# Performance work log

Hardware: AMD Instinct MI355X
Metric: run time of the kernel (lower is better)

The kernel has to match this reference:

```python
import jax, jax.numpy as jnp
import numpy as np

N_NODES = 50000
N_EDGES = 800000
IN_DIM = 128
HID_DIM = 256
OUT_DIM = 2


def setup_inputs() -> dict:
    key = jax.random.key(0)
    k = jax.random.split(key, 8)
    x = jax.random.normal(k[0], (N_NODES, IN_DIM), dtype=jnp.float32)
    edge_index = jax.random.randint(k[1], (2, N_EDGES), 0, N_NODES, dtype=jnp.int64)
    # Linear params (PyTorch-style fan-in scaling)
    W1 = jax.random.normal(k[2], (IN_DIM, HID_DIM), dtype=jnp.float32) / np.sqrt(IN_DIM)
    b1 = jnp.zeros((HID_DIM,), dtype=jnp.float32)
    W2 = jax.random.normal(k[3], (HID_DIM, OUT_DIM), dtype=jnp.float32) / np.sqrt(HID_DIM)
    b2 = jnp.zeros((OUT_DIM,), dtype=jnp.float32)
    # learnable GIN epsilons (init 0, as in PyG GINConv train_eps)
    eps1 = jnp.zeros((), dtype=jnp.float32)
    eps2 = jnp.zeros((), dtype=jnp.float32)
    return {"x": x, "edge_index": edge_index, "W1": W1, "b1": b1,
            "W2": W2, "b2": b2, "eps1": eps1, "eps2": eps2}


def _gin_conv(h, src, dst, num_nodes, eps, W, b):
    # aggregate: sum of neighbor features (scatter-add over edges)
    agg = jax.ops.segment_sum(h[src], dst, num_segments=num_nodes)  # [N, D]
    return ((1.0 + eps) * h + agg) @ W + b


def reference(x, edge_index, W1, b1, W2, b2, eps1, eps2):
    src, dst = edge_index[0], edge_index[1]
    n = x.shape[0]
    h = _gin_conv(x, src, dst, n, eps1, W1, b1)   # [N, HID]
    h = jax.nn.relu(h)
    out = _gin_conv(h, src, dst, n, eps2, W2, b2)  # [N, OUT]
    return out
```

## Files before the change

kernel.cpp:

```cpp
#include <hip/hip_runtime.h>

#define N_NODES 50000
#define N_EDGES 800000
#define IN_DIM 128
#define HID_DIM 256
#define OUT_DIM 2
#define CAP 64
#define NBKT 196
#define BCAP 6144
#define CHUNK 4096
#define POISON 0xAAAAAAAAu

typedef __attribute__((ext_vector_type(8))) short bh8;
typedef __attribute__((ext_vector_type(4))) float f4;
typedef __attribute__((ext_vector_type(4))) unsigned u4;

__device__ inline unsigned bf16rne(float f) {
    unsigned u = __float_as_uint(f);
    return (u + 0x7fffu + ((u >> 16) & 1u)) >> 16;
}
__device__ inline unsigned pack2(float lo, float hi) {
    return (bf16rne(hi) << 16) | bf16rne(lo);
}

__global__ __launch_bounds__(256) void k_prep_bin(
    const float* __restrict__ x, const float* __restrict__ W1,
    const int* __restrict__ ei,
    unsigned* __restrict__ xb, unsigned* __restrict__ W1p,
    unsigned* __restrict__ ccur, unsigned* __restrict__ coarse)
{
    __shared__ unsigned stage[CHUNK];
    __shared__ int hist[256], base[256], gpos[256], cur2[256];
    __shared__ int s_red[4];
    const int tid = threadIdx.x, lane = tid & 63, wv = tid >> 6;
    const int gtid = blockIdx.x * 256 + tid;
    const int gsz  = gridDim.x * 256;

    for (int i = gtid; i < 800000; i += gsz) {
        float4 a = ((const float4*)x)[2 * i];
        float4 b = ((const float4*)x)[2 * i + 1];
        u4 w;
        w[0] = pack2(a.x, a.y);
        w[1] = pack2(a.z, a.w);
        w[2] = pack2(b.x, b.y);
        w[3] = pack2(b.z, b.w);
        ((u4*)xb)[i] = w;
    }
    if (gtid < 16384) {
        int j = gtid;
        int d = j & 3, l = (j >> 2) & 63, s = (j >> 8) & 3, t = j >> 10;
        int k = 32 * s + 8 * (l >> 4) + 2 * d;
        int n = 16 * t + (l & 15);
        W1p[j] = (bf16rne(W1[(size_t)(k + 1) * HID_DIM + n]) << 16)
               |  bf16rne(W1[(size_t)k * HID_DIM + n]);
    }
    const int bid = blockIdx.x;
    if (bid >= NBKT) return;
    const int ebase = bid * CHUNK;
    const int ecnt  = min(CHUNK, N_EDGES - ebase);

    hist[tid] = 0;
    __syncthreads();
    int myd[16], mys[16];
#pragma unroll
    for (int r = 0; r < 16; r++) {
        int li = r * 256 + tid;
        if (li < ecnt) {
            int e = ebase + li;
            myd[r] = ei[N_EDGES + e];
            mys[r] = ei[e];
            atomicAdd(&hist[myd[r] >> 8], 1);
        } else myd[r] = -1;
    }
    __syncthreads();
    {
        int v = hist[tid], s = v;
#pragma unroll
        for (int off = 1; off < 64; off <<= 1) {
            int t = __shfl_up(s, off, 64);
            if (lane >= off) s += t;
        }
        if (lane == 63) s_red[wv] = s;
        __syncthreads();
        int wexcl = 0;
        for (int w = 0; w < wv; w++) wexcl += s_red[w];
        base[tid] = wexcl + s - v;
        cur2[tid] = 0;
        __syncthreads();
    }
    if (tid < NBKT && hist[tid] > 0) {
        atomicCAS(&ccur[tid], POISON, 0u);
        gpos[tid] = (int)atomicAdd(&ccur[tid], (unsigned)hist[tid]);
    }
    __syncthreads();
#pragma unroll
    for (int r = 0; r < 16; r++) {
        if (myd[r] >= 0) {
            int b = myd[r] >> 8;
            int pos = atomicAdd(&cur2[b], 1);
            stage[base[b] + pos] = ((unsigned)myd[r] << 16) | (unsigned)mys[r];
        }
    }
    __syncthreads();
    for (int i = tid; i < ecnt; i += 256) {
        unsigned rec = stage[i];
        int b = (int)(rec >> 24);
        int idx = gpos[b] + (i - base[b]);
        if (idx < BCAP) coarse[(size_t)b * BCAP + idx] = rec;
    }
}

__global__ __launch_bounds__(256) void k_fine(
    const unsigned* __restrict__ ccur, const unsigned* __restrict__ coarse,
    int* __restrict__ slots, int* __restrict__ cnt)
{
    __shared__ int cur[256];
    const int tid = threadIdx.x, bid = blockIdx.x;
    cur[tid] = 0;
    __syncthreads();
    const int cb = min((int)ccur[bid], BCAP);
    for (int i = tid; i < cb; i += 256) {
        unsigned rec = coarse[(size_t)bid * BCAP + i];
        int dst = (int)(rec >> 16);
        int src = (int)(rec & 0xffffu);
        int pos = atomicAdd(&cur[dst & 255], 1);
        if (pos < CAP) slots[(size_t)dst * CAP + pos] = src;
    }
    __syncthreads();
    int node = bid * 256 + tid;
    if (node < N_NODES) cnt[node] = min(cur[tid], CAP);
}

__global__ __launch_bounds__(256, 4) void k_gin1(
    const unsigned* __restrict__ xb,
    const int* __restrict__ cnt, const int* __restrict__ slots,
    const unsigned* __restrict__ W1p, const float* __restrict__ b1,
    const float* __restrict__ W2, const float* __restrict__ b2,
    const float* __restrict__ eps1p, const float* __restrict__ eps2p,
    float* __restrict__ p, float* __restrict__ out)
{
    __shared__ unsigned z[16 * 68];
    const int tid = threadIdx.x, lane = tid & 63, wv = tid >> 6;
    const int node0 = blockIdx.x * 16;
    const int nodeb = node0 + 4 * wv;
    const float e1 = 1.0f + eps1p[0];

    const int4 c4 = *(const int4*)(cnt + nodeb);
    int cns[4] = { min(c4.x, CAP), min(c4.y, CAP), min(c4.z, CAP), min(c4.w, CAP) };
    int srcs[4];
#pragma unroll
    for (int nn = 0; nn < 4; nn++) {
        srcs[nn] = slots[(size_t)(nodeb + nn) * CAP + ((lane < cns[nn]) ? lane : 0)];
    }
    unsigned us[4];
#pragma unroll
    for (int nn = 0; nn < 4; nn++)
        us[nn] = xb[(size_t)(nodeb + nn) * 64 + lane];
#pragma unroll
    for (int nn = 0; nn < 4; nn++)
        if (cns[nn] == 0) srcs[nn] = 0;

    unsigned u[4][16];
#pragma unroll
    for (int nn = 0; nn < 4; nn++) {
        int cn = cns[nn];
#pragma unroll
        for (int g = 0; g < 16; g++) {
            int sq = __shfl(srcs[nn], (g < cn) ? g : 0, 64);
            u[nn][g] = xb[(size_t)sq * 64 + lane];
        }
    }

#pragma unroll
    for (int nn = 0; nn < 4; nn++) {
        int cn = cns[nn];
        float ax = 0.f, ay = 0.f;
#pragma unroll
        for (int g = 0; g < 16; g++) {
            if (g < cn) {
                ax += __uint_as_float(u[nn][g] << 16);
                ay += __uint_as_float(u[nn][g] & 0xffff0000u);
            }
        }
        for (int j0 = 16; j0 < cn; j0 += 16) {
#pragma unroll
            for (int g = 0; g < 16; g++) {
                int idx = j0 + g;
                int sq = __shfl(srcs[nn], (idx < cn) ? idx : 0, 64);
                u[nn][g] = xb[(size_t)sq * 64 + lane];
            }
#pragma unroll
            for (int g = 0; g < 16; g++) {
                if (j0 + g < cn) {
                    ax += __uint_as_float(u[nn][g] << 16);
                    ay += __uint_as_float(u[nn][g] & 0xffff0000u);
                }
            }
        }
        ax = fmaf(e1, __uint_as_float(us[nn] << 16), ax);
        ay = fmaf(e1, __uint_as_float(us[nn] & 0xffff0000u), ay);
        z[(4 * wv + nn) * 68 + lane] = (bf16rne(ay) << 16) | bf16rne(ax);
    }
    __syncthreads();
    if (wv != 0) return;

    const int q = lane >> 4, c = lane & 15;
    bh8 afrag[4];
#pragma unroll
    for (int s = 0; s < 4; s++)
        afrag[s] = *(const bh8*)&z[c * 68 + 16 * s + 4 * q];

    f4 acc[16];
#pragma unroll
    for (int t = 0; t < 16; t++) acc[t] = (f4){0.f, 0.f, 0.f, 0.f};
#pragma unroll
    for (int t = 0; t < 16; t++) {
#pragma unroll
        for (int s = 0; s < 4; s++) {
            bh8 bfrag = *(const bh8*)(W1p + ((size_t)(t * 4 + s) * 64 + lane) * 4);
            acc[t] = __builtin_amdgcn_mfma_f32_16x16x32_bf16(afrag[s], bfrag, acc[t], 0, 0, 0);
        }
    }

    const float e2 = 1.0f + eps2p[0];
    float pxr[4] = {0.f, 0.f, 0.f, 0.f};
    float pyr[4] = {0.f, 0.f, 0.f, 0.f};
#pragma unroll
    for (int t = 0; t < 16; t++) {
        int n = 16 * t + c;
        float bb = b1[n];
        float2 w2 = *(const float2*)(W2 + (size_t)n * OUT_DIM);
#pragma unroll
        for (int r = 0; r < 4; r++) {
            float h = fmaxf(acc[t][r] + bb, 0.f);
            pxr[r] = fmaf(h, w2.x, pxr[r]);
            pyr[r] = fmaf(h, w2.y, pyr[r]);
        }
    }
#pragma unroll
    for (int off = 1; off < 16; off <<= 1) {
#pragma unroll
        for (int r = 0; r < 4; r++) {
            pxr[r] += __shfl_xor(pxr[r], off, 64);
            pyr[r] += __shfl_xor(pyr[r], off, 64);
        }
    }
    if (c == 0) {
        float2 b2v = *(const float2*)b2;
#pragma unroll
        for (int r = 0; r < 4; r++) {
            int node = node0 + q * 4 + r;
            *(float2*)(p + (size_t)node * OUT_DIM) = make_float2(pxr[r], pyr[r]);
            float2 o;
            o.x = fmaf(e2, pxr[r], b2v.x);
            o.y = fmaf(e2, pyr[r], b2v.y);
            *(float2*)(out + (size_t)node * OUT_DIM) = o;
        }
    }
}

__global__ __launch_bounds__(256) void k_out(
    const int* __restrict__ cnt, const int* __restrict__ slots,
    const float* __restrict__ p, float* __restrict__ out)
{
    const int tid = threadIdx.x, lane = tid & 63, wv = tid >> 6;
    const int node = blockIdx.x * 32 + wv * 8 + (lane >> 3);
    const int l = lane & 7;
    float sx = 0.f, sy = 0.f;
    if (node < N_NODES) {
        int cn = min(cnt[node], CAP);
        for (int j = l; j < cn; j += 8) {
            int src = slots[node * CAP + j];
            float2 v = *(const float2*)(p + (size_t)src * OUT_DIM);
            sx += v.x; sy += v.y;
        }
    }
#pragma unroll
    for (int off = 1; off <= 4; off <<= 1) {
        sx += __shfl_xor(sx, off, 64);
        sy += __shfl_xor(sy, off, 64);
    }
    if (l == 0 && node < N_NODES) {
        float2 o = *(const float2*)(out + (size_t)node * OUT_DIM);
        o.x += sx; o.y += sy;
        *(float2*)(out + (size_t)node * OUT_DIM) = o;
    }
}

extern "C" void kernel_launch(void* const* d_in, const int* in_sizes, int n_in,
                              void* d_out, int out_size, void* d_ws, size_t ws_size,
                              hipStream_t stream)
{
    (void)in_sizes; (void)n_in; (void)out_size; (void)ws_size;
    const float* x    = (const float*)d_in[0];
    const int*   ei   = (const int*)d_in[1];
    const float* W1   = (const float*)d_in[2];
    const float* b1   = (const float*)d_in[3];
    const float* W2   = (const float*)d_in[4];
    const float* b2   = (const float*)d_in[5];
    const float* eps1 = (const float*)d_in[6];
    const float* eps2 = (const float*)d_in[7];
    float* out = (float*)d_out;

    int* cnt         = (int*)d_ws;
    int* slots       = cnt + 50048;
    float* p         = (float*)(slots + 3200000);
    unsigned* xb     = (unsigned*)(p + 100000);
    unsigned* W1p    = xb + 3200000;
    unsigned* ccur   = (unsigned*)(W1p + 16384);
    unsigned* coarse = ccur + 256;

    k_prep_bin<<<2048, 256, 0, stream>>>(x, W1, ei, xb, W1p, ccur, coarse);
    k_fine<<<NBKT, 256, 0, stream>>>(ccur, coarse, slots, cnt);
    k_gin1<<<(N_NODES + 15) / 16, 256, 0, stream>>>(xb, cnt, slots,
                                                    W1p, b1, W2, b2,
                                                    eps1, eps2, p, out);
    k_out<<<(N_NODES + 31) / 32, 256, 0, stream>>>(cnt, slots, p, out);
}
```

Before: 173.3 us.

## Restructure GIN gather to 16-lane node groups and split MFMA across waves

The gather in k_gin1 now assigns 16 lanes per node, so each wave handles 4 nodes at once with 16-byte vector loads of the bf16 features, instead of looping over nodes with 4-byte loads per lane. The first-layer matmul is split so all four waves each compute a quarter of the hidden columns, rather than wave 0 doing all of it, and the partial second-layer projections are reduced through shared memory. k_fine switches to 1024-thread blocks and loads its bucket records into registers up front. Together these aim to raise memory-level parallelism in the gather and balance the matrix work across waves, at the cost of an extra block barrier and more register pressure.

```diff
diff --git a/kernel.cpp b/kernel.cpp
--- a/kernel.cpp
+++ b/kernel.cpp
@@ -110,25 +110,37 @@
     }
 }
 
-__global__ __launch_bounds__(256) void k_fine(
+__global__ __launch_bounds__(1024) void k_fine(
     const unsigned* __restrict__ ccur, const unsigned* __restrict__ coarse,
     int* __restrict__ slots, int* __restrict__ cnt)
 {
     __shared__ int cur[256];
     const int tid = threadIdx.x, bid = blockIdx.x;
-    cur[tid] = 0;
+    if (tid < 256) cur[tid] = 0;
     __syncthreads();
     const int cb = min((int)ccur[bid], BCAP);
-    for (int i = tid; i < cb; i += 256) {
-        unsigned rec = coarse[(size_t)bid * BCAP + i];
-        int dst = (int)(rec >> 16);
-        int src = (int)(rec & 0xffffu);
-        int pos = atomicAdd(&cur[dst & 255], 1);
-        if (pos < CAP) slots[(size_t)dst * CAP + pos] = src;
-    }
-    __syncthreads();
-    int node = bid * 256 + tid;
-    if (node < N_NODES) cnt[node] = min(cur[tid], CAP);
+    unsigned recs[6];
+#pragma unroll
+    for (int r = 0; r < 6; r++) {
+        int i = tid + r * 1024;
+        if (i < cb) recs[r] = coarse[(size_t)bid * BCAP + i];
+    }
+#pragma unroll
+    for (int r = 0; r < 6; r++) {
+        int i = tid + r * 1024;
+        if (i < cb) {
+            unsigned rec = recs[r];
+            int dst = (int)(rec >> 16);
+            int src = (int)(rec & 0xffffu);
+            int pos = atomicAdd(&cur[dst & 255], 1);
+            if (pos < CAP) slots[(size_t)dst * CAP + pos] = src;
+        }
+    }
+    __syncthreads();
+    if (tid < 256) {
+        int node = bid * 256 + tid;
+        if (node < N_NODES) cnt[node] = min(cur[tid], CAP);
+    }
 }
 
 __global__ __launch_bounds__(256, 4) void k_gin1(
@@ -139,70 +151,75 @@
     const float* __restrict__ eps1p, const float* __restrict__ eps2p,
     float* __restrict__ p, float* __restrict__ out)
 {
-    __shared__ unsigned z[16 * 68];
+    __shared__ __attribute__((aligned(16))) unsigned z[16 * 68];
+    __shared__ float2 pp[64];
     const int tid = threadIdx.x, lane = tid & 63, wv = tid >> 6;
     const int node0 = blockIdx.x * 16;
-    const int nodeb = node0 + 4 * wv;
+    const int sub = lane & 15;
+    const int grp = lane >> 4;
+    const int gb  = lane & 48;
+    const int node = node0 + 4 * wv + grp;
     const float e1 = 1.0f + eps1p[0];
-
-    const int4 c4 = *(const int4*)(cnt + nodeb);
-    int cns[4] = { min(c4.x, CAP), min(c4.y, CAP), min(c4.z, CAP), min(c4.w, CAP) };
-    int srcs[4];
-#pragma unroll
-    for (int nn = 0; nn < 4; nn++) {
-        srcs[nn] = slots[(size_t)(nodeb + nn) * CAP + ((lane < cns[nn]) ? lane : 0)];
-    }
-    unsigned us[4];
-#pragma unroll
-    for (int nn = 0; nn < 4; nn++)
-        us[nn] = xb[(size_t)(nodeb + nn) * 64 + lane];
-#pragma unroll
-    for (int nn = 0; nn < 4; nn++)
-        if (cns[nn] == 0) srcs[nn] = 0;
-
-    unsigned u[4][16];
-#pragma unroll
-    for (int nn = 0; nn < 4; nn++) {
-        int cn = cns[nn];
+    const u4* __restrict__ xb4 = (const u4*)xb;
+
+    const int cn = min(cnt[node], CAP);
+    int s1 = 0;
+    if (sub < cn) s1 = slots[(size_t)node * CAP + sub];
+
+    u4 us = xb4[(unsigned)(node * 16 + sub)];
+
+    u4 u[16];
+#pragma unroll
+    for (int g = 0; g < 16; g++) {
+        int sq = __shfl(s1, gb + g, 64);
+        u[g] = xb4[(unsigned)(sq * 16 + sub)];
+    }
+    float ax[8];
+#pragma unroll
+    for (int k = 0; k < 8; k++) ax[k] = 0.f;
+#pragma unroll
+    for (int g = 0; g < 16; g++) {
+        if (g < cn) {
+#pragma unroll
+            for (int k2 = 0; k2 < 4; k2++) {
+                unsigned w = u[g][k2];
+                ax[2 * k2]     += __uint_as_float(w << 16);
+                ax[2 * k2 + 1] += __uint_as_float(w & 0xffff0000u);
+            }
+        }
+    }
+    int j0 = 16;
+    while (__any(cn > j0)) {
+        int idx = j0 + sub;
+        int s2 = (idx < cn) ? slots[(size_t)node * CAP + idx] : 0;
+        u4 ut[16];
 #pragma unroll
         for (int g = 0; g < 16; g++) {
-            int sq = __shfl(srcs[nn], (g < cn) ? g : 0, 64);
-            u[nn][g] = xb[(size_t)sq * 64 + lane];
-        }
-    }
-
-#pragma unroll
-    for (int nn = 0; nn < 4; nn++) {
-        int cn = cns[nn];
-        float ax = 0.f, ay = 0.f;
+            int sq = __shfl(s2, gb + g, 64);
+            ut[g] = xb4[(unsigned)(sq * 16 + sub)];
+        }
 #pragma unroll
         for (int g = 0; g < 16; g++) {
-            if (g < cn) {
-                ax += __uint_as_float(u[nn][g] << 16);
-                ay += __uint_as_float(u[nn][g] & 0xffff0000u);
-            }
-        }
-        for (int j0 = 16; j0 < cn; j0 += 16) {
-#pragma unroll
-            for (int g = 0; g < 16; g++) {
-                int idx = j0 + g;
-                int sq = __shfl(srcs[nn], (idx < cn) ? idx : 0, 64);
-                u[nn][g] = xb[(size_t)sq * 64 + lane];
-            }
-#pragma unroll
-            for (int g = 0; g < 16; g++) {
-                if (j0 + g < cn) {
-                    ax += __uint_as_float(u[nn][g] << 16);
-                    ay += __uint_as_float(u[nn][g] & 0xffff0000u);
+            if (j0 + g < cn) {
+#pragma unroll
+                for (int k2 = 0; k2 < 4; k2++) {
+                    unsigned w = ut[g][k2];
+                    ax[2 * k2]     += __uint_as_float(w << 16);
+                    ax[2 * k2 + 1] += __uint_as_float(w & 0xffff0000u);
                 }
             }
         }
-        ax = fmaf(e1, __uint_as_float(us[nn] << 16), ax);
-        ay = fmaf(e1, __uint_as_float(us[nn] & 0xffff0000u), ay);
-        z[(4 * wv + nn) * 68 + lane] = (bf16rne(ay) << 16) | bf16rne(ax);
-    }
-    __syncthreads();
-    if (wv != 0) return;
+        j0 += 16;
+    }
+    u4 zw;
+#pragma unroll
+    for (int k2 = 0; k2 < 4; k2++) {
+        float lx = fmaf(e1, __uint_as_float(us[k2] << 16),         ax[2 * k2]);
+        float ly = fmaf(e1, __uint_as_float(us[k2] & 0xffff0000u), ax[2 * k2 + 1]);
+        zw[k2] = pack2(lx, ly);
+    }
+    *(u4*)&z[(4 * wv + grp) * 68 + 4 * sub] = zw;
+    __syncthreads();
 
     const int q = lane >> 4, c = lane & 15;
     bh8 afrag[4];
@@ -210,15 +227,16 @@
     for (int s = 0; s < 4; s++)
         afrag[s] = *(const bh8*)&z[c * 68 + 16 * s + 4 * q];
 
-    f4 acc[16];
-#pragma unroll
-    for (int t = 0; t < 16; t++) acc[t] = (f4){0.f, 0.f, 0.f, 0.f};
-#pragma unroll
-    for (int t = 0; t < 16; t++) {
+    f4 acc[4];
+#pragma unroll
+    for (int t = 0; t < 4; t++) acc[t] = (f4){0.f, 0.f, 0.f, 0.f};
+#pragma unroll
+    for (int tp = 0; tp < 4; tp++) {
+        int t = 4 * wv + tp;
 #pragma unroll
         for (int s = 0; s < 4; s++) {
             bh8 bfrag = *(const bh8*)(W1p + ((size_t)(t * 4 + s) * 64 + lane) * 4);
-            acc[t] = __builtin_amdgcn_mfma_f32_16x16x32_bf16(afrag[s], bfrag, acc[t], 0, 0, 0);
+            acc[tp] = __builtin_amdgcn_mfma_f32_16x16x32_bf16(afrag[s], bfrag, acc[tp], 0, 0, 0);
         }
     }
 
@@ -226,13 +244,13 @@
     float pxr[4] = {0.f, 0.f, 0.f, 0.f};
     float pyr[4] = {0.f, 0.f, 0.f, 0.f};
 #pragma unroll
-    for (int t = 0; t < 16; t++) {
-        int n = 16 * t + c;
+    for (int tp = 0; tp < 4; tp++) {
+        int n = 16 * (4 * wv + tp) + c;
         float bb = b1[n];
         float2 w2 = *(const float2*)(W2 + (size_t)n * OUT_DIM);
 #pragma unroll
         for (int r = 0; r < 4; r++) {
-            float h = fmaxf(acc[t][r] + bb, 0.f);
+            float h = fmaxf(acc[tp][r] + bb, 0.f);
             pxr[r] = fmaf(h, w2.x, pxr[r]);
             pyr[r] = fmaf(h, w2.y, pyr[r]);
         }
@@ -246,16 +264,26 @@
         }
     }
     if (c == 0) {
+#pragma unroll
+        for (int r = 0; r < 4; r++)
+            pp[wv * 16 + q * 4 + r] = make_float2(pxr[r], pyr[r]);
+    }
+    __syncthreads();
+
+    if (tid < 16) {
+        float px = 0.f, py = 0.f;
+#pragma unroll
+        for (int w = 0; w < 4; w++) {
+            float2 v = pp[w * 16 + tid];
+            px += v.x; py += v.y;
+        }
+        int nd = node0 + tid;
+        *(float2*)(p + (size_t)nd * OUT_DIM) = make_float2(px, py);
         float2 b2v = *(const float2*)b2;
-#pragma unroll
-        for (int r = 0; r < 4; r++) {
-            int node = node0 + q * 4 + r;
-            *(float2*)(p + (size_t)node * OUT_DIM) = make_float2(pxr[r], pyr[r]);
-            float2 o;
-            o.x = fmaf(e2, pxr[r], b2v.x);
-            o.y = fmaf(e2, pyr[r], b2v.y);
-            *(float2*)(out + (size_t)node * OUT_DIM) = o;
-        }
+        float2 o;
+        o.x = fmaf(e2, px, b2v.x);
+        o.y = fmaf(e2, py, b2v.y);
+        *(float2*)(out + (size_t)nd * OUT_DIM) = o;
     }
 }
 
@@ -311,7 +339,7 @@
     unsigned* coarse = ccur + 256;
 
     k_prep_bin<<<2048, 256, 0, stream>>>(x, W1, ei, xb, W1p, ccur, coarse);
-    k_fine<<<NBKT, 256, 0, stream>>>(ccur, coarse, slots, cnt);
+    k_fine<<<NBKT, 1024, 0, stream>>>(ccur, coarse, slots, cnt);
     k_gin1<<<(N_NODES + 15) / 16, 256, 0, stream>>>(xb, cnt, slots,
                                                     W1p, b1, W2, b2,
                                                     eps1, eps2, p, out);
```

After: 150.7 us. -13.0%, faster.
